# Optimization experiments

Measured on AMD Instinct MI355X. Metric: run time of the kernel, lower is better.

The kernel has to match this reference:

```python
import jax, jax.numpy as jnp
import numpy as np

GRID_SIZE, SPLINE_ORDER = 5, 3  # efficient-kan KANLinear defaults
NUM_BASES = GRID_SIZE + SPLINE_ORDER


def b_splines(x, grid):
    # x: (N, in_dim), grid: (in_dim, GRID_SIZE + 2*SPLINE_ORDER + 1)
    xe = x[..., None]
    bases = ((xe >= grid[:, :-1]) & (xe < grid[:, 1:])).astype(x.dtype)
    for k in range(1, SPLINE_ORDER + 1):  # Cox-de Boor recursion (static, 3 iters)
        left = (xe - grid[:, : -(k + 1)]) / (grid[:, k:-1] - grid[:, : -(k + 1)])
        right = (grid[:, k + 1:] - xe) / (grid[:, k + 1:] - grid[:, 1:-k])
        bases = left * bases[..., :-1] + right * bases[..., 1:]
    return bases  # (N, in_dim, NUM_BASES)


def kan_linear(x, grid, base_w, spline_w, scaler):
    # base branch: SiLU(x) @ W_base^T ; spline branch: B-spline basis @ scaled spline weights
    n = x.shape[0]
    out_dim = base_w.shape[0]
    base = jax.nn.silu(x) @ base_w.T
    bs = b_splines(x, grid).reshape(n, -1)                    # (N, in*NUM_BASES)
    sw = (spline_w * scaler[..., None]).reshape(out_dim, -1)  # (out, in*NUM_BASES)
    return base + bs @ sw.T


def setup_inputs() -> dict:
    key = jax.random.key(0)
    N, E, F, H, C, L = 50000, 500000, 128, 128, 40, 3
    ks = jax.random.split(key, 8)
    x = jax.random.normal(ks[0], (N, F), dtype=jnp.float32)
    edge_index = jax.random.randint(ks[1], (2, E), 0, N)
    # KAN grid (registered buffer in efficient-kan): uniform over [-1,1] extended by spline_order
    h_step = 2.0 / GRID_SIZE
    pts = np.arange(-SPLINE_ORDER, GRID_SIZE + SPLINE_ORDER + 1) * h_step - 1.0
    grid_mp = jnp.asarray(np.tile(pts, (F, 1)), dtype=jnp.float32)
    D = F + L * H  # skip-concat dim into output KANLinear
    grid_out = jnp.asarray(np.tile(pts, (D, 1)), dtype=jnp.float32)
    s = 0.1
    conv_base_w = jax.random.normal(ks[2], (L, H, F), dtype=jnp.float32) * s
    conv_spline_w = jax.random.normal(ks[3], (L, H, F, NUM_BASES), dtype=jnp.float32) * s
    conv_scaler = jnp.ones((L, H, F), dtype=jnp.float32)
    conv_bias = jnp.zeros((L, H), dtype=jnp.float32)
    bn_gamma = jnp.ones((L, H), dtype=jnp.float32)
    bn_beta = jnp.zeros((L, H), dtype=jnp.float32)
    out_base_w = jax.random.normal(ks[4], (C, D), dtype=jnp.float32) * s
    out_spline_w = jax.random.normal(ks[5], (C, D, NUM_BASES), dtype=jnp.float32) * s
    out_scaler = jnp.ones((C, D), dtype=jnp.float32)
    return dict(x=x, edge_index=edge_index, grid_mp=grid_mp, conv_base_w=conv_base_w,
                conv_spline_w=conv_spline_w, conv_scaler=conv_scaler, conv_bias=conv_bias,
                bn_gamma=bn_gamma, bn_beta=bn_beta, grid_out=grid_out,
                out_base_w=out_base_w, out_spline_w=out_spline_w, out_scaler=out_scaler)


def reference(x, edge_index, grid_mp, conv_base_w, conv_spline_w, conv_scaler, conv_bias,
              bn_gamma, bn_beta, grid_out, out_base_w, out_spline_w, out_scaler):
    N = x.shape[0]
    L = conv_base_w.shape[0]
    # GCN normalization with self-loops (computed once; identical each layer)
    loop = jnp.arange(N)
    src = jnp.concatenate([edge_index[0], loop])
    dst = jnp.concatenate([edge_index[1], loop])
    deg = jax.ops.segment_sum(jnp.ones_like(src, dtype=x.dtype), dst, num_segments=N)
    dinv = jnp.where(deg > 0, jax.lax.rsqrt(jnp.maximum(deg, 1.0)), 0.0)
    norm = dinv[src] * dinv[dst]  # (E+N,)
    feats = [x]
    for i in range(L):  # static layer loop
        h = kan_linear(x, grid_mp, conv_base_w[i], conv_spline_w[i], conv_scaler[i])
        # symmetric-normalized sparse aggregation (gather on src, scatter-add on dst)
        h = jax.ops.segment_sum(h[src] * norm[:, None], dst, num_segments=N) + conv_bias[i]
        # BatchNorm1d (training mode: biased batch statistics over nodes)
        mu = h.mean(axis=0)
        var = h.var(axis=0)
        x = (h - mu) * jax.lax.rsqrt(var + 1e-5) * bn_gamma[i] + bn_beta[i]
        feats.append(x)  # dropout p=0.0 is identity
    xc = jnp.concatenate(feats, axis=1)  # skip-concat: (N, F + L*H)
    logits = kan_linear(xc, grid_out, out_base_w, out_spline_w, out_scaler)
    return jax.nn.log_softmax(logits, axis=1)
```

## Files before the change

### kernel.cpp

```cpp
#include <hip/hip_runtime.h>
#include <hip/hip_bf16.h>
#include <math.h>

#define F_IN   128
#define HID    128
#define NLAYER 3
#define NCLS   40
#define DCAT   512
#define OOUT   64

typedef short s16x8 __attribute__((ext_vector_type(8)));
typedef unsigned short u16x8 __attribute__((ext_vector_type(8)));
typedef unsigned short u16x4 __attribute__((ext_vector_type(4)));
typedef float f32x4 __attribute__((ext_vector_type(4)));


static __device__ __forceinline__ float silu_f(float x) {
    return x / (1.f + __expf(-x));
}

static __device__ __forceinline__ unsigned short f2bf_rn(float f) {
    union { __hip_bfloat16 h; unsigned short u; } cv;
    cv.h = __float2bfloat16(f);
    return cv.u;
}

static __device__ __forceinline__ void gload_lds16(const void* g, void* l) {
    __builtin_amdgcn_global_load_lds(
        (const __attribute__((address_space(1))) void*)g,
        (__attribute__((address_space(3))) void*)l, 16, 0, 0);
}


__global__ __launch_bounds__(256) void deg_init_kernel(int* deg, int N) {
    for (int i = blockIdx.x * blockDim.x + threadIdx.x; i < N; i += gridDim.x * blockDim.x)
        deg[i] = 1;
}

__global__ __launch_bounds__(256) void deg_count_kernel(const int* __restrict__ dst, int E, int* deg) {
    for (int i = blockIdx.x * blockDim.x + threadIdx.x; i < E; i += gridDim.x * blockDim.x)
        atomicAdd(&deg[dst[i]], 1);
}

__global__ __launch_bounds__(256) void dinv_kernel(const int* __restrict__ deg, float* dinv, int N) {
    for (int i = blockIdx.x * blockDim.x + threadIdx.x; i < N; i += gridDim.x * blockDim.x)
        dinv[i] = rsqrtf((float)deg[i]);
}

__global__ __launch_bounds__(256) void scan_reduce_kernel(const int* __restrict__ deg, int* __restrict__ bsum, int N) {
    __shared__ int sh[256];
    int t = threadIdx.x;
    int e = blockIdx.x * 256 + t;
    sh[t] = (e < N) ? deg[e] : 0;
    __syncthreads();
#pragma unroll
    for (int off = 128; off > 0; off >>= 1) {
        if (t < off) sh[t] += sh[t + off];
        __syncthreads();
    }
    if (t == 0) bsum[blockIdx.x] = sh[0];
}

__global__ __launch_bounds__(256) void scan_top_kernel(const int* __restrict__ bsum, int* __restrict__ bbase, int nsb) {
    __shared__ int sh[256];
    int t = threadIdx.x;
    int chunk = (nsb + 255) >> 8;
    int begin = t * chunk;
    int end = begin + chunk; if (end > nsb) end = nsb;
    int s = 0;
    for (int i = begin; i < end; ++i) s += bsum[i];
    sh[t] = s;
    __syncthreads();
#pragma unroll
    for (int off = 1; off < 256; off <<= 1) {
        int v = 0;
        if (t >= off) v = sh[t - off];
        __syncthreads();
        if (t >= off) sh[t] += v;
        __syncthreads();
    }
    int run = (t == 0) ? 0 : sh[t - 1];
    for (int i = begin; i < end; ++i) {
        bbase[i] = run;
        run += bsum[i];
    }
}

__global__ __launch_bounds__(256) void scan_write_kernel(const int* __restrict__ deg,
                                                         const int* __restrict__ bbase,
                                                         int* __restrict__ offs, int* __restrict__ cursor, int N) {
    __shared__ int sh[256];
    int t = threadIdx.x;
    int e = blockIdx.x * 256 + t;
    int d = (e < N) ? deg[e] : 0;
    sh[t] = d;
    __syncthreads();
#pragma unroll
    for (int off = 1; off < 256; off <<= 1) {
        int v = 0;
        if (t >= off) v = sh[t - off];
        __syncthreads();
        if (t >= off) sh[t] += v;
        __syncthreads();
    }
    int incl = sh[t] + bbase[blockIdx.x];
    int excl = incl - d;
    if (e < N) {
        offs[e] = excl;
        cursor[e] = excl;
        if (e == N - 1) offs[N] = incl;
    }
}

__global__ __launch_bounds__(256) void fill_kernel(const int* __restrict__ src, const int* __restrict__ dst,
                                                   int E, int N, int* cursor, int* __restrict__ csr) {
    int total = E + N;
    for (int i = blockIdx.x * blockDim.x + threadIdx.x; i < total; i += gridDim.x * blockDim.x) {
        if (i < E) {
            int d = dst[i];
            int p = atomicAdd(&cursor[d], 1);
            csr[p] = src[i];
        } else {
            int n = i - E;
            int p = atomicAdd(&cursor[n], 1);
            csr[p] = n;
        }
    }
}

__global__ __launch_bounds__(256) void pack_conv_mfma(const float* __restrict__ bw,
                                                      const float* __restrict__ sw,
                                                      const float* __restrict__ sc,
                                                      unsigned short* __restrict__ wpk) {
    int total = NLAYER * 9 * 4 * 8 * 64 * 8;
    for (int idx = blockIdx.x * blockDim.x + threadIdx.x; idx < total; idx += gridDim.x * blockDim.x) {
        int e    = idx & 7;
        int lane = (idx >> 3) & 63;
        int cf   = (idx >> 9) & 7;
        int kk   = (idx >> 12) & 3;
        int cc   = (idx >> 14) % 9;
        int l    = idx / (9 << 14);
        int o = cf * 16 + (lane & 15);
        int k = kk * 32 + ((lane >> 4) << 3) + e;
        float v;
        if (cc == 8) {
            v = bw[(l * 128 + o) * 128 + k];
        } else {
            int f = cc * 16 + (k >> 3);
            int j = k & 7;
            int base = (l * 128 + o) * 128 + f;
            v = sw[base * 8 + j] * sc[base];
        }
        wpk[idx] = f2bf_rn(v);
    }
}

__global__ __launch_bounds__(256) void pack_out_mfma(const float* __restrict__ bw,
                                                     const float* __restrict__ sw,
                                                     const float* __restrict__ sc,
                                                     unsigned short* __restrict__ wpk) {
    int total = 36 * 4 * 4 * 64 * 8;
    for (int idx = blockIdx.x * blockDim.x + threadIdx.x; idx < total; idx += gridDim.x * blockDim.x) {
        int e    = idx & 7;
        int lane = (idx >> 3) & 63;
        int cf   = (idx >> 9) & 3;
        int kk   = (idx >> 11) & 3;
        int gcc  = idx >> 13;
        int g = gcc / 9, cc = gcc % 9;
        int o = cf * 16 + (lane & 15);
        int k = kk * 32 + ((lane >> 4) << 3) + e;
        float v = 0.f;
        if (o < NCLS) {
            if (cc == 8) {
                int f = g * 128 + k;
                v = bw[o * DCAT + f];
            } else {
                int f = g * 128 + cc * 16 + (k >> 3);
                int j = k & 7;
                int base = o * DCAT + f;
                v = sw[base * 8 + j] * sc[base];
            }
        }
        wpk[idx] = f2bf_rn(v);
    }
}


__global__ __launch_bounds__(256) void copyx_kernel(const float* __restrict__ x, float* __restrict__ xc, int N) {
    int total = N * F_IN;
    for (int idx = blockIdx.x * blockDim.x + threadIdx.x; idx < total; idx += gridDim.x * blockDim.x) {
        int n = idx >> 7, f = idx & 127;
        xc[(size_t)n * DCAT + f] = x[idx];
    }
}

__global__ __launch_bounds__(512) void affine_init_kernel(float* scA, float* shA) {
    int i = threadIdx.x;
    scA[i] = 1.f; shA[i] = 0.f;
}

template<bool CONV, bool INIT>
__global__ __launch_bounds__(256, 3) void kan_fused_kernel(
    const float* __restrict__ xc, int in_off,
    const float* __restrict__ scA, const float* __restrict__ shA,
    const unsigned short* __restrict__ wconv,
    const unsigned short* __restrict__ wout,
    unsigned short* __restrict__ silbuf,
    unsigned short* __restrict__ htmp,
    const float* __restrict__ dinv,
    float* __restrict__ out_acc, int N) {

    __shared__ __align__(16) char lds_phi[16384];

    const int tid = threadIdx.x;
    const int lane = tid & 63;
    const int wave = tid >> 6;
    const int l15 = lane & 15, lg = lane >> 4;
    const int nblk = blockIdx.x * 64;

    const float g0 = -1.f - 3.f * 0.4f;
    const float invh = 1.f / 0.4f;

    const int fg = tid & 3;
    const int n0 = tid >> 2;

    f32x4 accc[4][2];
    f32x4 acco[4];
    if (CONV) {
#pragma unroll
        for (int r = 0; r < 4; ++r)
#pragma unroll
            for (int c = 0; c < 2; ++c) accc[r][c] = (f32x4)0.f;
    }
#pragma unroll
    for (int r = 0; r < 4; ++r) acco[r] = (f32x4)0.f;

    float4 xq, scq, shq;
    auto ldx = [&](int cc) {
        int f0 = in_off + cc * 16 + fg * 4;
        scq = *(const float4*)(scA + f0);
        shq = *(const float4*)(shA + f0);
        int gn = nblk + n0;
        xq = (gn < N) ? *(const float4*)(xc + (size_t)gn * DCAT + f0) : (float4){0.f,0.f,0.f,0.f};
    };

    u16x8 pcur[4];
    auto phi_compute = [&](int ccc) {
        float xi[4] = {xq.x, xq.y, xq.z, xq.w};
        float scr[4] = {scq.x, scq.y, scq.z, scq.w};
        float shr[4] = {shq.x, shq.y, shq.z, shq.w};
        u16x4 sv;
#pragma unroll
        for (int fl = 0; fl < 4; ++fl) {
            float y = fmaf(xi[fl], scr[fl], shr[fl]);
            sv[fl] = f2bf_rn(silu_f(y));
            float t = (y - g0) * invh;
            float cf = floorf(t);
            int c = (int)cf;
            float u = t - cf;
            float um = 1.f - u;
            float u2 = u * u;
            float um2 = um * um;
            float w0 = um2 * um * (1.f / 6.f);
            float w3 = u2 * u * (1.f / 6.f);
            float w1 = fmaf(fmaf(0.5f, u, -1.f), u2, 2.f / 3.f);
            float w2 = fmaf(fmaf(-0.5f, u, 0.5f), u2, fmaf(0.5f, u, 1.f / 6.f));
            bool e[11];
#pragma unroll
            for (int v = 0; v < 11; ++v) e[v] = (c == v);
#pragma unroll
            for (int s = 0; s < 8; ++s) {
                float val = 0.f;
                val = e[s] ? w3 : val;
                val = e[s + 1] ? w2 : val;
                val = e[s + 2] ? w1 : val;
                val = e[s + 3] ? w0 : val;
                pcur[fl][s] = f2bf_rn(val);
            }
        }
        int gn = nblk + n0;
        if (gn < N) {
            int fdst = (ccc * 16 + fg * 4) ^ ((n0 & 7) << 3);
            *(u16x4*)(silbuf + (size_t)gn * 128 + fdst) = sv;
        }
    };

    auto mfma_phase = [&](const unsigned short* wcb, const unsigned short* wob) {
#pragma unroll
        for (int kk = 0; kk < 4; ++kk) {
            const int kb = kk * 64 + lg * 16;
            s16x8 af[4];
#pragma unroll
            for (int r = 0; r < 4; ++r) {
                int n = r * 16 + l15;
                af[r] = *(const s16x8*)(lds_phi + n * 256 + (kb ^ ((n & 7) << 4)));
            }
            if (CONV) {
#pragma unroll
                for (int c = 0; c < 2; ++c) {
                    int cf = wave * 2 + c;
                    s16x8 b = *(const s16x8*)(wcb + (((size_t)kk * 8 + cf) * 64 + lane) * 8);
#pragma unroll
                    for (int r = 0; r < 4; ++r)
                        accc[r][c] = __builtin_amdgcn_mfma_f32_16x16x32_bf16(af[r], b, accc[r][c], 0, 0, 0);
                }
            }
            {
                s16x8 b = *(const s16x8*)(wob + (((size_t)kk * 4 + wave) * 64 + lane) * 8);
#pragma unroll
                for (int r = 0; r < 4; ++r)
                    acco[r] = __builtin_amdgcn_mfma_f32_16x16x32_bf16(af[r], b, acco[r], 0, 0, 0);
            }
        }
    };

    ldx(0);
    phi_compute(0);

    for (int cc = 0; cc < 8; ++cc) {
        __syncthreads();
        {
            int swz = (n0 & 7) << 4;
#pragma unroll
            for (int i = 0; i < 4; ++i) {
                int byte = n0 * 256 + ((fg * 64 + i * 16) ^ swz);
                *(u16x8*)(lds_phi + byte) = pcur[i];
            }
        }
        __syncthreads();
        if (cc < 7) ldx(cc + 1);
        mfma_phase(CONV ? wconv + (size_t)cc * 16384 : nullptr, wout + (size_t)cc * 8192);
        if (cc < 7) phi_compute(cc + 1);
    }

    __syncthreads();
    {
        const unsigned short* ssrc = silbuf + (size_t)nblk * 128;
#pragma unroll
        for (int i = 0; i < 4; ++i) {
            int e = tid + i * 256;
            gload_lds16(ssrc + e * 8, lds_phi + e * 16);
        }
    }
    __syncthreads();
    mfma_phase(CONV ? wconv + (size_t)8 * 16384 : nullptr, wout + (size_t)8 * 8192);

#pragma unroll
    for (int r = 0; r < 4; ++r) {
        int nb = nblk + r * 16 + lg * 4;
        if (CONV) {
#pragma unroll
            for (int c = 0; c < 2; ++c) {
                int o = wave * 32 + c * 16 + l15;
#pragma unroll
                for (int q = 0; q < 4; ++q) {
                    int n = nb + q;
                    if (n < N) htmp[(size_t)n * HID + o] = f2bf_rn(accc[r][c][q] * dinv[n]);
                }
            }
        }
        {
            int o = wave * 16 + l15;
            if (o < NCLS) {
#pragma unroll
                for (int q = 0; q < 4; ++q) {
                    int n = nb + q;
                    if (n < N) {
                        size_t a = (size_t)n * OOUT + o;
                        float v = acco[r][q];
                        if (!INIT) v += out_acc[a];
                        out_acc[a] = v;
                    }
                }
            }
        }
    }
}

__global__ __launch_bounds__(256) void agg_kernel(const unsigned short* __restrict__ h,
                                                  const float* __restrict__ dinv,
                                                  const int* __restrict__ offs,
                                                  const int* __restrict__ csr,
                                                  const float* __restrict__ bias,
                                                  float* __restrict__ xc, int out_off, int N) {
    int n = blockIdx.x * 4 + (threadIdx.x >> 6);
    if (n >= N) return;
    int lane = threadIdx.x & 63;
    int s = offs[n], e = offs[n + 1];
    float a0 = 0.f, a1 = 0.f, b0 = 0.f, b1 = 0.f;
    float c0 = 0.f, c1 = 0.f, d0 = 0.f, d1 = 0.f;
    int i = s;
    for (; i + 4 <= e; i += 4) {
        int v0 = csr[i], v1 = csr[i + 1], v2 = csr[i + 2], v3 = csr[i + 3];
        unsigned u0 = *(const unsigned*)(h + (size_t)v0 * HID + lane * 2);
        unsigned u1 = *(const unsigned*)(h + (size_t)v1 * HID + lane * 2);
        unsigned u2 = *(const unsigned*)(h + (size_t)v2 * HID + lane * 2);
        unsigned u3 = *(const unsigned*)(h + (size_t)v3 * HID + lane * 2);
        a0 += __uint_as_float(u0 << 16);
        a1 += __uint_as_float(u0 & 0xffff0000u);
        b0 += __uint_as_float(u1 << 16);
        b1 += __uint_as_float(u1 & 0xffff0000u);
        c0 += __uint_as_float(u2 << 16);
        c1 += __uint_as_float(u2 & 0xffff0000u);
        d0 += __uint_as_float(u3 << 16);
        d1 += __uint_as_float(u3 & 0xffff0000u);
    }
    for (; i < e; ++i) {
        int v = csr[i];
        unsigned u = *(const unsigned*)(h + (size_t)v * HID + lane * 2);
        a0 += __uint_as_float(u << 16);
        a1 += __uint_as_float(u & 0xffff0000u);
    }
    a0 += b0 + c0 + d0;
    a1 += b1 + c1 + d1;
    float dn = dinv[n];
    float2 bv = *(const float2*)(bias + lane * 2);
    float2 res = {fmaf(a0, dn, bv.x), fmaf(a1, dn, bv.y)};
    *(float2*)(xc + (size_t)n * DCAT + out_off + lane * 2) = res;
}

__global__ __launch_bounds__(128) void bn_stats_kernel(const float* __restrict__ xc, int off, int N,
                                                       float* __restrict__ bnsum, float* __restrict__ bnsq) {
    int f = threadIdx.x;
    float s = 0.f, q = 0.f;
    for (int n = blockIdx.x; n < N; n += gridDim.x) {
        float v = xc[(size_t)n * DCAT + off + f];
        s += v;
        q += v * v;
    }
    atomicAdd(&bnsum[f], s);
    atomicAdd(&bnsq[f], q);
}

__global__ __launch_bounds__(128) void bn_affine_kernel(const float* __restrict__ bnsum,
                                                        const float* __restrict__ bnsq,
                                                        const float* __restrict__ gamma,
                                                        const float* __restrict__ beta,
                                                        float* scA, float* shA, int seg_off, float invN) {
    int f = threadIdx.x;
    float mu = bnsum[f] * invN;
    float var = bnsq[f] * invN - mu * mu;
    float rs = rsqrtf(var + 1e-5f);
    float s = gamma[f] * rs;
    scA[seg_off + f] = s;
    shA[seg_off + f] = fmaf(-mu, s, beta[f]);
}

__global__ __launch_bounds__(256) void logsoftmax_kernel(const float* __restrict__ oacc,
                                                         float* __restrict__ out, int N) {
    for (int n = blockIdx.x * blockDim.x + threadIdx.x; n < N; n += gridDim.x * blockDim.x) {
        const float* row = oacc + (size_t)n * OOUT;
        float m = -1e30f;
#pragma unroll
        for (int j = 0; j < NCLS; ++j) m = fmaxf(m, row[j]);
        float s = 0.f;
#pragma unroll
        for (int j = 0; j < NCLS; ++j) s += __expf(row[j] - m);
        float lse = m + __logf(s);
        float* orow = out + (size_t)n * NCLS;
#pragma unroll
        for (int j = 0; j < NCLS; ++j) orow[j] = row[j] - lse;
    }
}


extern "C" void kernel_launch(void* const* d_in, const int* in_sizes, int n_in,
                              void* d_out, int out_size, void* d_ws, size_t ws_size,
                              hipStream_t stream) {
    const float* x            = (const float*)d_in[0];
    const int*   eidx         = (const int*)d_in[1];
    const float* conv_base_w  = (const float*)d_in[3];
    const float* conv_spline_w= (const float*)d_in[4];
    const float* conv_scaler  = (const float*)d_in[5];
    const float* conv_bias    = (const float*)d_in[6];
    const float* bn_gamma     = (const float*)d_in[7];
    const float* bn_beta      = (const float*)d_in[8];
    const float* out_base_w   = (const float*)d_in[10];
    const float* out_spline_w = (const float*)d_in[11];
    const float* out_scaler   = (const float*)d_in[12];
    float* out = (float*)d_out;

    int N = in_sizes[0] / F_IN;
    int E = in_sizes[1] / 2;
    const int* esrc = eidx;
    const int* edst = eidx + E;

    int blocks = (N + 63) / 64;
    int npad = blocks * 64;
    int nsb = (N + 255) / 256;

    char* p = (char*)d_ws;
    auto carve = [&](size_t bytes) {
        char* r = p;
        p += (bytes + 255) & ~(size_t)255;
        return r;
    };
    float* xc   = (float*)carve((size_t)N * DCAT * 4);
    unsigned short* htmp = (unsigned short*)carve((size_t)npad * HID * 2);
    float* oacc = (float*)carve((size_t)npad * OOUT * 4);
    unsigned short* silbuf = (unsigned short*)carve((size_t)npad * 128 * 2);
    float* dinv = (float*)carve((size_t)N * 4);
    float* bn   = (float*)carve((size_t)NLAYER * 2 * HID * 4);
    float* scA  = (float*)carve((size_t)DCAT * 4);
    float* shA  = (float*)carve((size_t)DCAT * 4);
    unsigned short* wpkc = (unsigned short*)carve((size_t)NLAYER * 9 * 128 * 128 * 2);
    unsigned short* wpko = (unsigned short*)carve((size_t)36 * 64 * 128 * 2);
    int* deg    = (int*)carve((size_t)N * 4);
    int* offs   = (int*)carve((size_t)(N + 1) * 4);
    int* cursor = (int*)carve((size_t)(N + 1) * 4);
    int* bsum   = (int*)carve((size_t)nsb * 4);
    int* bbase  = (int*)carve((size_t)nsb * 4);
    int* csr    = (int*)carve((size_t)(E + N) * 4);

    hipMemsetAsync(bn, 0, NLAYER * 2 * HID * 4, stream);

    deg_init_kernel<<<512, 256, 0, stream>>>(deg, N);
    deg_count_kernel<<<1024, 256, 0, stream>>>(edst, E, deg);
    dinv_kernel<<<512, 256, 0, stream>>>(deg, dinv, N);
    scan_reduce_kernel<<<nsb, 256, 0, stream>>>(deg, bsum, N);
    scan_top_kernel<<<1, 256, 0, stream>>>(bsum, bbase, nsb);
    scan_write_kernel<<<nsb, 256, 0, stream>>>(deg, bbase, offs, cursor, N);
    fill_kernel<<<1024, 256, 0, stream>>>(esrc, edst, E, N, cursor, csr);

    pack_conv_mfma<<<1024, 256, 0, stream>>>(conv_base_w, conv_spline_w, conv_scaler, wpkc);
    pack_out_mfma<<<1024, 256, 0, stream>>>(out_base_w, out_spline_w, out_scaler, wpko);
    copyx_kernel<<<2048, 256, 0, stream>>>(x, xc, N);
    affine_init_kernel<<<1, 512, 0, stream>>>(scA, shA);

    float invN = 1.f / (float)N;
    for (int l = 0; l < NLAYER; ++l) {
        int in_off = l * HID;
        int out_off = (l + 1) * HID;
        const unsigned short* wl = wpkc + (size_t)l * 9 * 16384;
        const unsigned short* wo = wpko + (size_t)l * 9 * 8192;
        if (l == 0)
            kan_fused_kernel<true, true><<<blocks, 256, 0, stream>>>(
                xc, in_off, scA, shA, wl, wo, silbuf, htmp, dinv, oacc, N);
        else
            kan_fused_kernel<true, false><<<blocks, 256, 0, stream>>>(
                xc, in_off, scA, shA, wl, wo, silbuf, htmp, dinv, oacc, N);
        agg_kernel<<<(N + 3) / 4, 256, 0, stream>>>(htmp, dinv, offs, csr, conv_bias + l * HID, xc, out_off, N);
        float* bnsum = bn + l * 2 * HID;
        float* bnsq  = bnsum + HID;
        bn_stats_kernel<<<256, 128, 0, stream>>>(xc, out_off, N, bnsum, bnsq);
        bn_affine_kernel<<<1, 128, 0, stream>>>(bnsum, bnsq, bn_gamma + l * HID, bn_beta + l * HID,
                                                scA, shA, out_off, invN);
    }

    kan_fused_kernel<false, false><<<blocks, 256, 0, stream>>>(
        xc, 384, scA, shA, nullptr, wpko + (size_t)3 * 9 * 8192, silbuf, nullptr, dinv, oacc, N);

    logsoftmax_kernel<<<(N + 255) / 256, 256, 0, stream>>>(oacc, out, N);
}
```

Baseline: 590.8 us.

## Double-buffer KAN phi tiles in LDS and prefetch weight fragments into registers

The fused KAN kernel now uses two LDS phi buffers, so computing and writing the next chunk's B-spline basis overlaps with the MFMA phase on the current chunk. This cuts the barriers per iteration from two to one. The next chunk's weight fragments and x/scale/shift values are prefetched into registers ahead of use, replacing global loads inside the MFMA loop. In exchange, LDS and register use go up, and the occupancy hint drops from 3 to 2 blocks per CU, which reduces latency hiding across waves.

```diff
diff --git a/kernel.cpp b/kernel.cpp
--- a/kernel.cpp
+++ b/kernel.cpp
@@ -200,7 +200,7 @@
 }
 
 template<bool CONV, bool INIT>
-__global__ __launch_bounds__(256, 3) void kan_fused_kernel(
+__global__ __launch_bounds__(256, 2) void kan_fused_kernel(
     const float* __restrict__ xc, int in_off,
     const float* __restrict__ scA, const float* __restrict__ shA,
     const unsigned short* __restrict__ wconv,
@@ -210,7 +210,8 @@
     const float* __restrict__ dinv,
     float* __restrict__ out_acc, int N) {
 
-    __shared__ __align__(16) char lds_phi[16384];
+    __shared__ __align__(16) char lds_phi0[16384];
+    __shared__ __align__(16) char lds_phi1[16384];
 
     const int tid = threadIdx.x;
     const int lane = tid & 63;
@@ -235,20 +236,39 @@
 #pragma unroll
     for (int r = 0; r < 4; ++r) acco[r] = (f32x4)0.f;
 
-    float4 xq, scq, shq;
-    auto ldx = [&](int cc) {
+    float4 xqb[2], scb[2], shb[2];
+    auto ldx = [&](int cc, int slot) {
         int f0 = in_off + cc * 16 + fg * 4;
-        scq = *(const float4*)(scA + f0);
-        shq = *(const float4*)(shA + f0);
+        scb[slot] = *(const float4*)(scA + f0);
+        shb[slot] = *(const float4*)(shA + f0);
         int gn = nblk + n0;
-        xq = (gn < N) ? *(const float4*)(xc + (size_t)gn * DCAT + f0) : (float4){0.f,0.f,0.f,0.f};
+        xqb[slot] = (gn < N) ? *(const float4*)(xc + (size_t)gn * DCAT + f0) : (float4){0.f,0.f,0.f,0.f};
     };
 
+    s16x8 wc_reg[4][2];
+    s16x8 wo_reg[4];
+    auto loadW = [&](int cc) {
+        if (CONV) {
+            const unsigned short* wcb = wconv + (size_t)cc * 16384;
+#pragma unroll
+            for (int kk = 0; kk < 4; ++kk)
+#pragma unroll
+                for (int c = 0; c < 2; ++c) {
+                    int cf = wave * 2 + c;
+                    wc_reg[kk][c] = *(const s16x8*)(wcb + (((size_t)kk * 8 + cf) * 64 + lane) * 8);
+                }
+        }
+        const unsigned short* wob = wout + (size_t)cc * 8192;
+#pragma unroll
+        for (int kk = 0; kk < 4; ++kk)
+            wo_reg[kk] = *(const s16x8*)(wob + (((size_t)kk * 4 + wave) * 64 + lane) * 8);
+    };
+
     u16x8 pcur[4];
-    auto phi_compute = [&](int ccc) {
-        float xi[4] = {xq.x, xq.y, xq.z, xq.w};
-        float scr[4] = {scq.x, scq.y, scq.z, scq.w};
-        float shr[4] = {shq.x, shq.y, shq.z, shq.w};
+    auto phi_compute = [&](int ccc, int slot) {
+        float xi[4] = {xqb[slot].x, xqb[slot].y, xqb[slot].z, xqb[slot].w};
+        float scr[4] = {scb[slot].x, scb[slot].y, scb[slot].z, scb[slot].w};
+        float shr[4] = {shb[slot].x, shb[slot].y, shb[slot].z, shb[slot].w};
         u16x4 sv;
 #pragma unroll
         for (int fl = 0; fl < 4; ++fl) {
@@ -285,7 +305,16 @@
         }
     };
 
-    auto mfma_phase = [&](const unsigned short* wcb, const unsigned short* wob) {
+    auto write_phi = [&](char* buf) {
+        int swz = (n0 & 7) << 4;
+#pragma unroll
+        for (int i = 0; i < 4; ++i) {
+            int byte = n0 * 256 + ((fg * 64 + i * 16) ^ swz);
+            *(u16x8*)(buf + byte) = pcur[i];
+        }
+    };
+
+    auto mfma_phase = [&](const char* buf) {
 #pragma unroll
         for (int kk = 0; kk < 4; ++kk) {
             const int kb = kk * 64 + lg * 16;
@@ -293,57 +322,49 @@
 #pragma unroll
             for (int r = 0; r < 4; ++r) {
                 int n = r * 16 + l15;
-                af[r] = *(const s16x8*)(lds_phi + n * 256 + (kb ^ ((n & 7) << 4)));
+                af[r] = *(const s16x8*)(buf + n * 256 + (kb ^ ((n & 7) << 4)));
             }
             if (CONV) {
 #pragma unroll
-                for (int c = 0; c < 2; ++c) {
-                    int cf = wave * 2 + c;
-                    s16x8 b = *(const s16x8*)(wcb + (((size_t)kk * 8 + cf) * 64 + lane) * 8);
+                for (int c = 0; c < 2; ++c)
 #pragma unroll
                     for (int r = 0; r < 4; ++r)
-                        accc[r][c] = __builtin_amdgcn_mfma_f32_16x16x32_bf16(af[r], b, accc[r][c], 0, 0, 0);
-                }
-            }
-            {
-                s16x8 b = *(const s16x8*)(wob + (((size_t)kk * 4 + wave) * 64 + lane) * 8);
-#pragma unroll
-                for (int r = 0; r < 4; ++r)
-                    acco[r] = __builtin_amdgcn_mfma_f32_16x16x32_bf16(af[r], b, acco[r], 0, 0, 0);
-            }
+                        accc[r][c] = __builtin_amdgcn_mfma_f32_16x16x32_bf16(af[r], wc_reg[kk][c], accc[r][c], 0, 0, 0);
+            }
+#pragma unroll
+            for (int r = 0; r < 4; ++r)
+                acco[r] = __builtin_amdgcn_mfma_f32_16x16x32_bf16(af[r], wo_reg[kk], acco[r], 0, 0, 0);
         }
     };
 
-    ldx(0);
-    phi_compute(0);
-
-    for (int cc = 0; cc < 8; ++cc) {
-        __syncthreads();
-        {
-            int swz = (n0 & 7) << 4;
+    ldx(0, 0);
+    phi_compute(0, 0);
+    ldx(1, 1);
+    loadW(0);
+    write_phi(lds_phi0);
+    __syncthreads();
+
+#pragma unroll
+    for (int cc = 0; cc < 9; ++cc) {
+        char* cur = (cc & 1) ? lds_phi1 : lds_phi0;
+        char* nxt = (cc & 1) ? lds_phi0 : lds_phi1;
+        mfma_phase(cur);
+        if (cc < 8) loadW(cc + 1);
+        if (cc < 7) {
+            ldx(cc + 2, cc & 1);
+            phi_compute(cc + 1, (cc + 1) & 1);
+            write_phi(nxt);
+        }
+        if (cc == 7) {
+            const unsigned short* ssrc = silbuf + (size_t)nblk * 128;
 #pragma unroll
             for (int i = 0; i < 4; ++i) {
-                int byte = n0 * 256 + ((fg * 64 + i * 16) ^ swz);
-                *(u16x8*)(lds_phi + byte) = pcur[i];
-            }
-        }
-        __syncthreads();
-        if (cc < 7) ldx(cc + 1);
-        mfma_phase(CONV ? wconv + (size_t)cc * 16384 : nullptr, wout + (size_t)cc * 8192);
-        if (cc < 7) phi_compute(cc + 1);
-    }
-
-    __syncthreads();
-    {
-        const unsigned short* ssrc = silbuf + (size_t)nblk * 128;
-#pragma unroll
-        for (int i = 0; i < 4; ++i) {
-            int e = tid + i * 256;
-            gload_lds16(ssrc + e * 8, lds_phi + e * 16);
-        }
-    }
-    __syncthreads();
-    mfma_phase(CONV ? wconv + (size_t)8 * 16384 : nullptr, wout + (size_t)8 * 8192);
+                int e = tid + i * 256;
+                gload_lds16(ssrc + e * 8, nxt + e * 16);
+            }
+        }
+        if (cc < 8) __syncthreads();
+    }
 
 #pragma unroll
     for (int r = 0; r < 4; ++r) {
```

Measured after the change: 545.5 us. 7.7% less time.
